# Kernel tuning notes

Measured on AMD Instinct MI355X. Metric: run time of the kernel, lower is better.

Reference implementation:

```python
import jax, jax.numpy as jnp
import numpy as np
import math

B, T, D_MODEL, H = 2, 2048, 768, 12
D = D_MODEL // H
EPS = 1e-8


def _l2norm(x, eps=EPS):
    # torch.nn.functional.normalize: x / max(||x||, eps)
    n = jnp.sqrt(jnp.sum(x * x, axis=-1, keepdims=True))
    return x / jnp.maximum(n, eps)


def setup_inputs() -> dict:
    key = jax.random.key(0)
    ks = jax.random.split(key, 7)
    sc = 1.0 / math.sqrt(D_MODEL)
    inp = {
        "query": jax.random.normal(ks[0], (B, T, D_MODEL), jnp.float32),
        "key": jax.random.normal(ks[1], (B, T, D_MODEL), jnp.float32),
        "value": jax.random.normal(ks[2], (B, T, D_MODEL), jnp.float32),
        "Wq": jax.random.normal(ks[3], (D_MODEL, D_MODEL), jnp.float32) * sc,
        "Wk": jax.random.normal(ks[4], (D_MODEL, D_MODEL), jnp.float32) * sc,
        "Wv": jax.random.normal(ks[5], (D_MODEL, D_MODEL), jnp.float32) * sc,
        "Wo": jax.random.normal(ks[6], (D_MODEL, D_MODEL), jnp.float32) * sc,
        "s_v": jnp.linspace(0.0, math.log(255.0), H).astype(jnp.float32),
        "s_r": jnp.zeros((H,), jnp.float32),
    }
    return inp


def reference(query, key, value, Wq, Wk, Wv, Wo, s_v, s_r):
    b, t, _ = query.shape

    def proj(x, W):  # Linear(bias=False) then split heads -> [B,H,T,D]
        return (x @ W.T).reshape(b, t, H, D).transpose(0, 2, 1, 3)

    q = _l2norm(proj(query, Wq))
    k = _l2norm(proj(key, Wk))
    v = _l2norm(proj(value, Wv))

    w = jnp.exp(s_v) + 1.0  # per-head decay exponent, in [2, 256]
    r = jnp.exp(s_r) + 1.0  # per-head scale

    # cosine-similarity scores in [-1, 1]
    s = jnp.einsum("bhqd,bhkd->bhqk", q, k)
    base = jnp.clip((s + 1.0) * 0.5, 0.0, 1.0)
    alpha = r[None, :, None, None] * jnp.power(base, w[None, :, None, None])

    # causal mask (no softmax normalization in screening attention)
    causal = jnp.tril(jnp.ones((t, t), dtype=bool))
    alpha = jnp.where(causal[None, None], alpha, 0.0)

    out = jnp.einsum("bhqk,bhkd->bhqd", alpha, v)  # [B,H,T,D]

    # TanhNorm: bound magnitude along head dim via tanh of the norm
    n = jnp.sqrt(jnp.sum(out * out, axis=-1, keepdims=True))
    out = jnp.tanh(n) * out / (n + EPS)

    out = out.transpose(0, 2, 1, 3).reshape(b, t, D_MODEL)
    return out @ Wo.T
```

## Files before the change

### kernel.cpp

```cpp
#include <hip/hip_runtime.h>
#include <hip/hip_bf16.h>
#include <math.h>


typedef __attribute__((ext_vector_type(8))) short short8;
typedef __attribute__((ext_vector_type(4))) float f32x4;
typedef __attribute__((ext_vector_type(4))) unsigned int uint4v;
typedef __attribute__((ext_vector_type(2))) unsigned int uint2v;
typedef __attribute__((ext_vector_type(4))) float float4v;

#define MFMA_BF16(a, b, c) __builtin_amdgcn_mfma_f32_16x16x32_bf16((a), (b), (c), 0, 0, 0)

static __device__ __forceinline__ unsigned short f2bf(float f) {
  union { float f; unsigned u; } v; v.f = f;
  unsigned r = v.u + 0x7FFFu + ((v.u >> 16) & 1u);
  return (unsigned short)(r >> 16);
}
static __device__ __forceinline__ unsigned pack2(float a, float b) {
  return (unsigned)f2bf(a) | ((unsigned)f2bf(b) << 16);
}
static __device__ __forceinline__ void gload_lds16(const void* g, void* l) {
  __builtin_amdgcn_global_load_lds((const __attribute__((address_space(1))) unsigned int*)g,
                                   (__attribute__((address_space(3))) unsigned int*)l, 16, 0, 0);
}

__global__ __launch_bounds__(256) void k_cvt(
    const float* __restrict__ s0, const float* __restrict__ s1, const float* __restrict__ s2,
    const float* __restrict__ s3, const float* __restrict__ s4, const float* __restrict__ s5,
    const float* __restrict__ s6, unsigned short* __restrict__ dst) {
  const size_t e = ((size_t)blockIdx.x * 256 + threadIdx.x) * 8;
  const float* src;
  size_t off;
  if (e < 9437184) {
    const int i = (int)(e / 3145728);
    src = (i == 0) ? s0 : (i == 1) ? s1 : s2;
    off = e - (size_t)i * 3145728;
  } else {
    const size_t ew = e - 9437184;
    const int i = (int)(ew / 589824);
    src = (i == 0) ? s3 : (i == 1) ? s4 : (i == 2) ? s5 : s6;
    off = ew - (size_t)i * 589824;
  }
  const float4v f0 = *(const float4v*)(src + off);
  const float4v f1 = *(const float4v*)(src + off + 4);
  uint4v u = {pack2(f0.x, f0.y), pack2(f0.z, f0.w), pack2(f1.x, f1.y), pack2(f1.z, f1.w)};
  *(uint4v*)(dst + e) = u;
}

__global__ __launch_bounds__(256) void k_proj(
    const unsigned short* __restrict__ Xb, const unsigned short* __restrict__ Wb,
    unsigned short* __restrict__ qb, unsigned short* __restrict__ kb,
    unsigned short* __restrict__ vtb) {
  __shared__ alignas(16) unsigned char smem[49152];
  float* o_s = (float*)smem;
  unsigned short* vt_s = (unsigned short*)smem;

  const int which = blockIdx.z;
  const int h = blockIdx.y;
  const unsigned short* X = Xb + (size_t)which * 3145728;
  const unsigned short* W = Wb + (size_t)which * 589824 + (size_t)h * 64 * 768;

  const int mbase = blockIdx.x * 128;
  const int tid = threadIdx.x;
  const int lane = tid & 63;
  const int wv = tid >> 6;
  const int wm = wv >> 1, wn = wv & 1;
  const int l15 = lane & 15, l4 = lane >> 4;
  const int srow8 = lane >> 3;
  const int schunk = (lane & 7) ^ srow8;

  f32x4 acc[4][2];
#pragma unroll
  for (int m = 0; m < 4; ++m)
#pragma unroll
    for (int n = 0; n < 2; ++n) acc[m][n] = (f32x4){0.f, 0.f, 0.f, 0.f};

#pragma unroll
  for (int i = 0; i < 4; ++i) {
    const int j = wv * 4 + i;
    gload_lds16(X + (size_t)(mbase + j * 8 + srow8) * 768 + schunk * 8, smem + j * 1024);
  }
#pragma unroll
  for (int i = 0; i < 2; ++i) {
    const int j = wv * 2 + i;
    gload_lds16(W + (size_t)(j * 8 + srow8) * 768 + schunk * 8, smem + 16384 + j * 1024);
  }

  for (int ks = 0; ks < 12; ++ks) {
    const int cur = (ks & 1) * 24576;
    asm volatile("s_waitcnt vmcnt(0)" ::: "memory");
    __builtin_amdgcn_sched_barrier(0);
    __builtin_amdgcn_s_barrier();
    __builtin_amdgcn_sched_barrier(0);
    if (ks < 11) {
      const int nxt = ((ks + 1) & 1) * 24576;
      const int k0n = (ks + 1) * 64;
#pragma unroll
      for (int i = 0; i < 4; ++i) {
        const int j = wv * 4 + i;
        gload_lds16(X + (size_t)(mbase + j * 8 + srow8) * 768 + k0n + schunk * 8,
                    smem + nxt + j * 1024);
      }
#pragma unroll
      for (int i = 0; i < 2; ++i) {
        const int j = wv * 2 + i;
        gload_lds16(W + (size_t)(j * 8 + srow8) * 768 + k0n + schunk * 8,
                    smem + nxt + 16384 + j * 1024);
      }
      __builtin_amdgcn_sched_barrier(0);
    }
    __builtin_amdgcn_s_setprio(1);
#pragma unroll
    for (int kc = 0; kc < 2; ++kc) {
      const int cx = (kc << 2) | l4;
      short8 ar[4], br[2];
#pragma unroll
      for (int m = 0; m < 4; ++m) {
        const int r = wm * 64 + m * 16 + l15;
        ar[m] = *(const short8*)(smem + cur + r * 128 + ((cx ^ (r & 7)) << 4));
      }
#pragma unroll
      for (int n = 0; n < 2; ++n) {
        const int r = wn * 32 + n * 16 + l15;
        br[n] = *(const short8*)(smem + cur + 16384 + r * 128 + ((cx ^ (r & 7)) << 4));
      }
#pragma unroll
      for (int m = 0; m < 4; ++m)
#pragma unroll
        for (int n = 0; n < 2; ++n) acc[m][n] = MFMA_BF16(ar[m], br[n], acc[m][n]);
    }
    __builtin_amdgcn_s_setprio(0);
  }

  const int b = mbase >> 11;
  const int tbase = mbase & 2047;
  const int bh = b * 12 + h;
  __syncthreads();
#pragma unroll
  for (int m = 0; m < 4; ++m)
#pragma unroll
    for (int n = 0; n < 2; ++n)
#pragma unroll
      for (int j = 0; j < 4; ++j)
        o_s[(wm * 64 + m * 16 + l4 * 4 + j) * 68 + wn * 32 + n * 16 + l15] = acc[m][n][j];
  __syncthreads();
  const int row2 = tid >> 1, half = tid & 1;
  float v[32];
  float ss = 0.f;
#pragma unroll
  for (int c = 0; c < 8; ++c) {
    float4v f = *(const float4v*)(o_s + row2 * 68 + half * 32 + c * 4);
    v[c * 4 + 0] = f.x; v[c * 4 + 1] = f.y; v[c * 4 + 2] = f.z; v[c * 4 + 3] = f.w;
    ss += f.x * f.x + f.y * f.y + f.z * f.z + f.w * f.w;
  }
  ss += __shfl_xor(ss, 1);
  const float inv = 1.f / fmaxf(sqrtf(ss), 1e-8f);
  if (which < 2) {
    unsigned short* outp =
        ((which == 0) ? qb : kb) + ((size_t)bh * 2048 + tbase + row2) * 64 + half * 32;
#pragma unroll
    for (int c = 0; c < 4; ++c) {
      uint4v o = {pack2(v[c * 8 + 0] * inv, v[c * 8 + 1] * inv),
                  pack2(v[c * 8 + 2] * inv, v[c * 8 + 3] * inv),
                  pack2(v[c * 8 + 4] * inv, v[c * 8 + 5] * inv),
                  pack2(v[c * 8 + 6] * inv, v[c * 8 + 7] * inv)};
      *(uint4v*)(outp + c * 8) = o;
    }
  } else {
    __syncthreads();
#pragma unroll
    for (int c = 0; c < 32; ++c)
      vt_s[(half * 32 + c) * 136 + row2] = f2bf(v[c] * inv);
    __syncthreads();
    const int d = tid >> 2, tc = (tid & 3) * 32;
    unsigned short* dst = vtb + ((size_t)bh * 64 + d) * 2048 + tbase + tc;
#pragma unroll
    for (int c = 0; c < 4; ++c)
      *(uint4v*)(dst + c * 8) = *(const uint4v*)(vt_s + d * 136 + tc + c * 8);
  }
}

__global__ __launch_bounds__(256) void k_attn(
    const unsigned short* __restrict__ qb, const unsigned short* __restrict__ kb,
    const unsigned short* __restrict__ vtb, const float* __restrict__ s_v,
    const float* __restrict__ s_r, unsigned short* __restrict__ attn) {
  __shared__ alignas(16) unsigned char smem[41984];
  unsigned short* p_s = (unsigned short*)(smem + 32768);
  float* o_s = (float*)smem;

  const int bid = blockIdx.x;
  const int ii = bid & 255, jj = bid >> 8;
  const int rank = (jj == 0) ? ii : (jj == 1) ? (511 - ii) : (512 + ii);
  const int qt = 31 - (rank / 24);
  const int bh = rank % 24;
  const int b = bh / 12, h = bh % 12;
  const int qbase = qt * 64;
  const unsigned short* Qp = qb + (size_t)bh * 2048 * 64;
  const unsigned short* Kp = kb + (size_t)bh * 2048 * 64;
  const unsigned short* VTp = vtb + (size_t)bh * 64 * 2048;

  const int tid = threadIdx.x;
  const int lane = tid & 63;
  const int wv = tid >> 6;
  const int wm = wv >> 1, wn = wv & 1;
  const int l15 = lane & 15, l4 = lane >> 4;
  const int srow8 = lane >> 3;
  const int schunk = (lane & 7) ^ srow8;

  const float w_h = expf(s_v[h]) + 1.0f;
  const float lr_h = log2f(expf(s_r[h]) + 1.0f);

#pragma unroll
  for (int i = 0; i < 2; ++i) {
    const int j = wv * 2 + i;
    gload_lds16(Kp + (size_t)(j * 8 + srow8) * 64 + schunk * 8, smem + j * 1024);
    gload_lds16(VTp + (size_t)(j * 8 + srow8) * 2048 + schunk * 8, smem + 16384 + j * 1024);
  }

  short8 qf[2][2];
#pragma unroll
  for (int n = 0; n < 2; ++n)
#pragma unroll
    for (int kc = 0; kc < 2; ++kc)
      qf[n][kc] = *(const short8*)(Qp + (size_t)(qbase + wn * 32 + n * 16 + l15) * 64 + kc * 32 +
                                   l4 * 8);

  f32x4 acc_o[2][2];
#pragma unroll
  for (int m = 0; m < 2; ++m)
#pragma unroll
    for (int n = 0; n < 2; ++n) acc_o[m][n] = (f32x4){0.f, 0.f, 0.f, 0.f};

  for (int kt = 0; kt <= qt; ++kt) {
    const int cur = (kt & 1) * 8192;
    asm volatile("s_waitcnt vmcnt(0)" ::: "memory");
    __builtin_amdgcn_sched_barrier(0);
    __builtin_amdgcn_s_barrier();
    __builtin_amdgcn_sched_barrier(0);
    if (kt < qt) {
      const int nxt = ((kt + 1) & 1) * 8192;
      const int kb2 = (kt + 1) * 64;
#pragma unroll
      for (int i = 0; i < 2; ++i) {
        const int j = wv * 2 + i;
        gload_lds16(Kp + (size_t)(kb2 + j * 8 + srow8) * 64 + schunk * 8, smem + nxt + j * 1024);
        gload_lds16(VTp + (size_t)(j * 8 + srow8) * 2048 + kb2 + schunk * 8,
                    smem + 16384 + nxt + j * 1024);
      }
      __builtin_amdgcn_sched_barrier(0);
    }
    f32x4 s_acc[2][2];
#pragma unroll
    for (int m = 0; m < 2; ++m)
#pragma unroll
      for (int n = 0; n < 2; ++n) s_acc[m][n] = (f32x4){0.f, 0.f, 0.f, 0.f};
    __builtin_amdgcn_s_setprio(1);
#pragma unroll
    for (int kc = 0; kc < 2; ++kc) {
      const int cx = (kc << 2) | l4;
      const int r0 = wm * 32 + l15, r1 = wm * 32 + 16 + l15;
      short8 a0 = *(const short8*)(smem + cur + r0 * 128 + ((cx ^ (r0 & 7)) << 4));
      short8 a1 = *(const short8*)(smem + cur + r1 * 128 + ((cx ^ (r1 & 7)) << 4));
      s_acc[0][0] = MFMA_BF16(a0, qf[0][kc], s_acc[0][0]);
      s_acc[0][1] = MFMA_BF16(a0, qf[1][kc], s_acc[0][1]);
      s_acc[1][0] = MFMA_BF16(a1, qf[0][kc], s_acc[1][0]);
      s_acc[1][1] = MFMA_BF16(a1, qf[1][kc], s_acc[1][1]);
    }
    __builtin_amdgcn_s_setprio(0);
    const bool diag = (kt == qt);
#pragma unroll
    for (int m = 0; m < 2; ++m)
#pragma unroll
      for (int n = 0; n < 2; ++n) {
        const int lkb = wm * 32 + m * 16 + l4 * 4;
        const int lq = wn * 32 + n * 16 + l15;
        float av[4];
#pragma unroll
        for (int t = 0; t < 4; ++t) {
          const float base = __builtin_amdgcn_fmed3f(fmaf(s_acc[m][n][t], 0.5f, 0.5f), 0.f, 1.f);
          float a = __builtin_amdgcn_exp2f(fmaf(w_h, __builtin_amdgcn_logf(base), lr_h));
          if (diag && (lkb + t) > lq) a = 0.f;
          av[t] = a;
        }
        uint2v u = {pack2(av[0], av[1]), pack2(av[2], av[3])};
        *(uint2v*)(p_s + lq * 72 + lkb) = u;
      }
    asm volatile("s_waitcnt lgkmcnt(0)" ::: "memory");
    __builtin_amdgcn_sched_barrier(0);
    __builtin_amdgcn_s_barrier();
    __builtin_amdgcn_sched_barrier(0);
    __builtin_amdgcn_s_setprio(1);
#pragma unroll
    for (int kc = 0; kc < 2; ++kc) {
      const int cx = (kc << 2) | l4;
      const int r0 = wm * 32 + l15, r1 = wm * 32 + 16 + l15;
      short8 pa0 = *(const short8*)(p_s + (wn * 32 + l15) * 72 + kc * 32 + l4 * 8);
      short8 pa1 = *(const short8*)(p_s + (wn * 32 + 16 + l15) * 72 + kc * 32 + l4 * 8);
      short8 vb0 = *(const short8*)(smem + 16384 + cur + r0 * 128 + ((cx ^ (r0 & 7)) << 4));
      short8 vb1 = *(const short8*)(smem + 16384 + cur + r1 * 128 + ((cx ^ (r1 & 7)) << 4));
      acc_o[0][0] = MFMA_BF16(pa0, vb0, acc_o[0][0]);
      acc_o[0][1] = MFMA_BF16(pa0, vb1, acc_o[0][1]);
      acc_o[1][0] = MFMA_BF16(pa1, vb0, acc_o[1][0]);
      acc_o[1][1] = MFMA_BF16(pa1, vb1, acc_o[1][1]);
    }
    __builtin_amdgcn_s_setprio(0);
  }
  __syncthreads();
#pragma unroll
  for (int qi = 0; qi < 2; ++qi)
#pragma unroll
    for (int di = 0; di < 2; ++di)
#pragma unroll
      for (int j = 0; j < 4; ++j)
        o_s[(wn * 32 + qi * 16 + l4 * 4 + j) * 68 + wm * 32 + di * 16 + l15] = acc_o[qi][di][j];
  __syncthreads();
  {
    const int row = tid >> 2, q4 = tid & 3;
    float vals[16];
    float ss = 0.f;
#pragma unroll
    for (int j = 0; j < 16; ++j) {
      vals[j] = o_s[row * 68 + q4 * 16 + j];
      ss += vals[j] * vals[j];
    }
    ss += __shfl_xor(ss, 1);
    ss += __shfl_xor(ss, 2);
    const float nrm = sqrtf(ss);
    const float sc = tanhf(nrm) / (nrm + 1e-8f);
    unsigned short* dst = attn + (size_t)(b * 2048 + qbase + row) * 768 + h * 64 + q4 * 16;
    uint4v o0 = {pack2(vals[0] * sc, vals[1] * sc), pack2(vals[2] * sc, vals[3] * sc),
                 pack2(vals[4] * sc, vals[5] * sc), pack2(vals[6] * sc, vals[7] * sc)};
    uint4v o1 = {pack2(vals[8] * sc, vals[9] * sc), pack2(vals[10] * sc, vals[11] * sc),
                 pack2(vals[12] * sc, vals[13] * sc), pack2(vals[14] * sc, vals[15] * sc)};
    *(uint4v*)(dst) = o0;
    *(uint4v*)(dst + 8) = o1;
  }
}

__global__ __launch_bounds__(256) void k_outproj(const unsigned short* __restrict__ attn,
                                                 const unsigned short* __restrict__ Wob,
                                                 float* __restrict__ out) {
  __shared__ alignas(16) unsigned char smem[49152];
  const int mbase = blockIdx.x * 128;
  const int nbase = blockIdx.y * 64;
  const int tid = threadIdx.x;
  const int lane = tid & 63;
  const int wv = tid >> 6;
  const int wm = wv >> 1, wn = wv & 1;
  const int l15 = lane & 15, l4 = lane >> 4;
  const int srow8 = lane >> 3;
  const int schunk = (lane & 7) ^ srow8;

  f32x4 acc[4][2];
#pragma unroll
  for (int m = 0; m < 4; ++m)
#pragma unroll
    for (int n = 0; n < 2; ++n) acc[m][n] = (f32x4){0.f, 0.f, 0.f, 0.f};

#pragma unroll
  for (int i = 0; i < 4; ++i) {
    const int j = wv * 4 + i;
    gload_lds16(attn + (size_t)(mbase + j * 8 + srow8) * 768 + schunk * 8, smem + j * 1024);
  }
#pragma unroll
  for (int i = 0; i < 2; ++i) {
    const int j = wv * 2 + i;
    gload_lds16(Wob + (size_t)(nbase + j * 8 + srow8) * 768 + schunk * 8,
                smem + 16384 + j * 1024);
  }

  for (int ks = 0; ks < 12; ++ks) {
    const int cur = (ks & 1) * 24576;
    asm volatile("s_waitcnt vmcnt(0)" ::: "memory");
    __builtin_amdgcn_sched_barrier(0);
    __builtin_amdgcn_s_barrier();
    __builtin_amdgcn_sched_barrier(0);
    if (ks < 11) {
      const int nxt = ((ks + 1) & 1) * 24576;
      const int k0n = (ks + 1) * 64;
#pragma unroll
      for (int i = 0; i < 4; ++i) {
        const int j = wv * 4 + i;
        gload_lds16(attn + (size_t)(mbase + j * 8 + srow8) * 768 + k0n + schunk * 8,
                    smem + nxt + j * 1024);
      }
#pragma unroll
      for (int i = 0; i < 2; ++i) {
        const int j = wv * 2 + i;
        gload_lds16(Wob + (size_t)(nbase + j * 8 + srow8) * 768 + k0n + schunk * 8,
                    smem + nxt + 16384 + j * 1024);
      }
      __builtin_amdgcn_sched_barrier(0);
    }
    __builtin_amdgcn_s_setprio(1);
#pragma unroll
    for (int kc = 0; kc < 2; ++kc) {
      const int cx = (kc << 2) | l4;
      short8 ar[4], br[2];
#pragma unroll
      for (int m = 0; m < 4; ++m) {
        const int r = wm * 64 + m * 16 + l15;
        ar[m] = *(const short8*)(smem + cur + r * 128 + ((cx ^ (r & 7)) << 4));
      }
#pragma unroll
      for (int n = 0; n < 2; ++n) {
        const int r = wn * 32 + n * 16 + l15;
        br[n] = *(const short8*)(smem + cur + 16384 + r * 128 + ((cx ^ (r & 7)) << 4));
      }
#pragma unroll
      for (int m = 0; m < 4; ++m)
#pragma unroll
        for (int n = 0; n < 2; ++n) acc[m][n] = MFMA_BF16(ar[m], br[n], acc[m][n]);
    }
    __builtin_amdgcn_s_setprio(0);
  }
#pragma unroll
  for (int m = 0; m < 4; ++m)
#pragma unroll
    for (int n = 0; n < 2; ++n)
#pragma unroll
      for (int j = 0; j < 4; ++j)
        out[(size_t)(mbase + wm * 64 + m * 16 + l4 * 4 + j) * 768 + nbase + wn * 32 + n * 16 +
            l15] = acc[m][n][j];
}

extern "C" void kernel_launch(void* const* d_in, const int* in_sizes, int n_in, void* d_out,
                              int out_size, void* d_ws, size_t ws_size, hipStream_t stream) {
  (void)in_sizes;
  (void)n_in;
  (void)out_size;
  (void)ws_size;
  const float* query = (const float*)d_in[0];
  const float* key = (const float*)d_in[1];
  const float* value = (const float*)d_in[2];
  const float* Wq = (const float*)d_in[3];
  const float* Wk = (const float*)d_in[4];
  const float* Wv = (const float*)d_in[5];
  const float* Wo = (const float*)d_in[6];
  const float* s_v = (const float*)d_in[7];
  const float* s_r = (const float*)d_in[8];
  float* out = (float*)d_out;

  unsigned short* cvt = (unsigned short*)d_ws;
  unsigned short* Xb = cvt;
  unsigned short* Wb = cvt + 9437184;
  unsigned short* qb = cvt + 11796480;
  unsigned short* kb = qb + 3145728;
  unsigned short* vtb = kb + 3145728;
  unsigned short* attn = cvt;

  k_cvt<<<5760, 256, 0, stream>>>(query, key, value, Wq, Wk, Wv, Wo, cvt);
  k_proj<<<dim3(32, 12, 3), 256, 0, stream>>>(Xb, Wb, qb, kb, vtb);
  k_attn<<<dim3(768), 256, 0, stream>>>(qb, kb, vtb, s_v, s_r, attn);
  k_outproj<<<dim3(32, 12), 256, 0, stream>>>(attn, Wb + 3 * 589824, out);
}
```

Baseline: 82.63 us.

## Split attention tile across eight waves instead of four

Raises the attention kernel block from 256 to 512 threads and gives each wave a 32x16 sub-tile instead of 32x32, so every wave issues half as many MFMAs and exp/log evaluations per key tile. The goal is more waves per CU, to hide LDS and exp latency and shorten the serial per-block chain on the causal workload. The cost is more barrier participants, lower per-wave reuse of K/V fragments loaded from LDS, and a different epilogue split (eight threads per row with an extra shuffle).

```diff
diff --git a/kernel.cpp b/kernel.cpp
--- a/kernel.cpp
+++ b/kernel.cpp
@@ -180,7 +180,7 @@
   }
 }
 
-__global__ __launch_bounds__(256) void k_attn(
+__global__ __launch_bounds__(512) void k_attn(
     const unsigned short* __restrict__ qb, const unsigned short* __restrict__ kb,
     const unsigned short* __restrict__ vtb, const float* __restrict__ s_v,
     const float* __restrict__ s_r, unsigned short* __restrict__ attn) {
@@ -202,7 +202,7 @@
   const int tid = threadIdx.x;
   const int lane = tid & 63;
   const int wv = tid >> 6;
-  const int wm = wv >> 1, wn = wv & 1;
+  const int wm = wv >> 2, wn = wv & 3;
   const int l15 = lane & 15, l4 = lane >> 4;
   const int srow8 = lane >> 3;
   const int schunk = (lane & 7) ^ srow8;
@@ -210,26 +210,17 @@
   const float w_h = expf(s_v[h]) + 1.0f;
   const float lr_h = log2f(expf(s_r[h]) + 1.0f);
 
-#pragma unroll
-  for (int i = 0; i < 2; ++i) {
-    const int j = wv * 2 + i;
-    gload_lds16(Kp + (size_t)(j * 8 + srow8) * 64 + schunk * 8, smem + j * 1024);
-    gload_lds16(VTp + (size_t)(j * 8 + srow8) * 2048 + schunk * 8, smem + 16384 + j * 1024);
-  }
-
-  short8 qf[2][2];
-#pragma unroll
-  for (int n = 0; n < 2; ++n)
-#pragma unroll
-    for (int kc = 0; kc < 2; ++kc)
-      qf[n][kc] = *(const short8*)(Qp + (size_t)(qbase + wn * 32 + n * 16 + l15) * 64 + kc * 32 +
-                                   l4 * 8);
-
-  f32x4 acc_o[2][2];
-#pragma unroll
-  for (int m = 0; m < 2; ++m)
-#pragma unroll
-    for (int n = 0; n < 2; ++n) acc_o[m][n] = (f32x4){0.f, 0.f, 0.f, 0.f};
+  gload_lds16(Kp + (size_t)(wv * 8 + srow8) * 64 + schunk * 8, smem + wv * 1024);
+  gload_lds16(VTp + (size_t)(wv * 8 + srow8) * 2048 + schunk * 8, smem + 16384 + wv * 1024);
+
+  short8 qf[2];
+#pragma unroll
+  for (int kc = 0; kc < 2; ++kc)
+    qf[kc] = *(const short8*)(Qp + (size_t)(qbase + wn * 16 + l15) * 64 + kc * 32 + l4 * 8);
+
+  f32x4 acc_o[2];
+#pragma unroll
+  for (int m = 0; m < 2; ++m) acc_o[m] = (f32x4){0.f, 0.f, 0.f, 0.f};
 
   for (int kt = 0; kt <= qt; ++kt) {
     const int cur = (kt & 1) * 8192;
@@ -240,20 +231,14 @@
     if (kt < qt) {
       const int nxt = ((kt + 1) & 1) * 8192;
       const int kb2 = (kt + 1) * 64;
-#pragma unroll
-      for (int i = 0; i < 2; ++i) {
-        const int j = wv * 2 + i;
-        gload_lds16(Kp + (size_t)(kb2 + j * 8 + srow8) * 64 + schunk * 8, smem + nxt + j * 1024);
-        gload_lds16(VTp + (size_t)(j * 8 + srow8) * 2048 + kb2 + schunk * 8,
-                    smem + 16384 + nxt + j * 1024);
-      }
+      gload_lds16(Kp + (size_t)(kb2 + wv * 8 + srow8) * 64 + schunk * 8, smem + nxt + wv * 1024);
+      gload_lds16(VTp + (size_t)(wv * 8 + srow8) * 2048 + kb2 + schunk * 8,
+                  smem + 16384 + nxt + wv * 1024);
       __builtin_amdgcn_sched_barrier(0);
     }
-    f32x4 s_acc[2][2];
-#pragma unroll
-    for (int m = 0; m < 2; ++m)
-#pragma unroll
-      for (int n = 0; n < 2; ++n) s_acc[m][n] = (f32x4){0.f, 0.f, 0.f, 0.f};
+    f32x4 s_acc[2];
+#pragma unroll
+    for (int m = 0; m < 2; ++m) s_acc[m] = (f32x4){0.f, 0.f, 0.f, 0.f};
     __builtin_amdgcn_s_setprio(1);
 #pragma unroll
     for (int kc = 0; kc < 2; ++kc) {
@@ -261,30 +246,26 @@
       const int r0 = wm * 32 + l15, r1 = wm * 32 + 16 + l15;
       short8 a0 = *(const short8*)(smem + cur + r0 * 128 + ((cx ^ (r0 & 7)) << 4));
       short8 a1 = *(const short8*)(smem + cur + r1 * 128 + ((cx ^ (r1 & 7)) << 4));
-      s_acc[0][0] = MFMA_BF16(a0, qf[0][kc], s_acc[0][0]);
-      s_acc[0][1] = MFMA_BF16(a0, qf[1][kc], s_acc[0][1]);
-      s_acc[1][0] = MFMA_BF16(a1, qf[0][kc], s_acc[1][0]);
-      s_acc[1][1] = MFMA_BF16(a1, qf[1][kc], s_acc[1][1]);
+      s_acc[0] = MFMA_BF16(a0, qf[kc], s_acc[0]);
+      s_acc[1] = MFMA_BF16(a1, qf[kc], s_acc[1]);
     }
     __builtin_amdgcn_s_setprio(0);
     const bool diag = (kt == qt);
 #pragma unroll
-    for (int m = 0; m < 2; ++m)
-#pragma unroll
-      for (int n = 0; n < 2; ++n) {
-        const int lkb = wm * 32 + m * 16 + l4 * 4;
-        const int lq = wn * 32 + n * 16 + l15;
-        float av[4];
-#pragma unroll
-        for (int t = 0; t < 4; ++t) {
-          const float base = __builtin_amdgcn_fmed3f(fmaf(s_acc[m][n][t], 0.5f, 0.5f), 0.f, 1.f);
-          float a = __builtin_amdgcn_exp2f(fmaf(w_h, __builtin_amdgcn_logf(base), lr_h));
-          if (diag && (lkb + t) > lq) a = 0.f;
-          av[t] = a;
-        }
-        uint2v u = {pack2(av[0], av[1]), pack2(av[2], av[3])};
-        *(uint2v*)(p_s + lq * 72 + lkb) = u;
-      }
+    for (int m = 0; m < 2; ++m) {
+      const int lkb = wm * 32 + m * 16 + l4 * 4;
+      const int lq = wn * 16 + l15;
+      float av[4];
+#pragma unroll
+      for (int t = 0; t < 4; ++t) {
+        const float base = __builtin_amdgcn_fmed3f(fmaf(s_acc[m][t], 0.5f, 0.5f), 0.f, 1.f);
+        float a = __builtin_amdgcn_exp2f(fmaf(w_h, __builtin_amdgcn_logf(base), lr_h));
+        if (diag && (lkb + t) > lq) a = 0.f;
+        av[t] = a;
+      }
+      uint2v u = {pack2(av[0], av[1]), pack2(av[2], av[3])};
+      *(uint2v*)(p_s + lq * 72 + lkb) = u;
+    }
     asm volatile("s_waitcnt lgkmcnt(0)" ::: "memory");
     __builtin_amdgcn_sched_barrier(0);
     __builtin_amdgcn_s_barrier();
@@ -294,46 +275,40 @@
     for (int kc = 0; kc < 2; ++kc) {
       const int cx = (kc << 2) | l4;
       const int r0 = wm * 32 + l15, r1 = wm * 32 + 16 + l15;
-      short8 pa0 = *(const short8*)(p_s + (wn * 32 + l15) * 72 + kc * 32 + l4 * 8);
-      short8 pa1 = *(const short8*)(p_s + (wn * 32 + 16 + l15) * 72 + kc * 32 + l4 * 8);
+      short8 pa = *(const short8*)(p_s + (wn * 16 + l15) * 72 + kc * 32 + l4 * 8);
       short8 vb0 = *(const short8*)(smem + 16384 + cur + r0 * 128 + ((cx ^ (r0 & 7)) << 4));
       short8 vb1 = *(const short8*)(smem + 16384 + cur + r1 * 128 + ((cx ^ (r1 & 7)) << 4));
-      acc_o[0][0] = MFMA_BF16(pa0, vb0, acc_o[0][0]);
-      acc_o[0][1] = MFMA_BF16(pa0, vb1, acc_o[0][1]);
-      acc_o[1][0] = MFMA_BF16(pa1, vb0, acc_o[1][0]);
-      acc_o[1][1] = MFMA_BF16(pa1, vb1, acc_o[1][1]);
+      acc_o[0] = MFMA_BF16(pa, vb0, acc_o[0]);
+      acc_o[1] = MFMA_BF16(pa, vb1, acc_o[1]);
     }
     __builtin_amdgcn_s_setprio(0);
   }
   __syncthreads();
 #pragma unroll
-  for (int qi = 0; qi < 2; ++qi)
-#pragma unroll
-    for (int di = 0; di < 2; ++di)
-#pragma unroll
-      for (int j = 0; j < 4; ++j)
-        o_s[(wn * 32 + qi * 16 + l4 * 4 + j) * 68 + wm * 32 + di * 16 + l15] = acc_o[qi][di][j];
+  for (int m = 0; m < 2; ++m)
+#pragma unroll
+    for (int j = 0; j < 4; ++j)
+      o_s[(wn * 16 + l4 * 4 + j) * 68 + wm * 32 + m * 16 + l15] = acc_o[m][j];
   __syncthreads();
   {
-    const int row = tid >> 2, q4 = tid & 3;
-    float vals[16];
+    const int row = tid >> 3, d8 = (tid & 7) * 8;
+    float vals[8];
     float ss = 0.f;
 #pragma unroll
-    for (int j = 0; j < 16; ++j) {
-      vals[j] = o_s[row * 68 + q4 * 16 + j];
-      ss += vals[j] * vals[j];
+    for (int c = 0; c < 2; ++c) {
+      float4v f = *(const float4v*)(o_s + row * 68 + d8 + c * 4);
+      vals[c * 4 + 0] = f.x; vals[c * 4 + 1] = f.y; vals[c * 4 + 2] = f.z; vals[c * 4 + 3] = f.w;
+      ss += f.x * f.x + f.y * f.y + f.z * f.z + f.w * f.w;
     }
     ss += __shfl_xor(ss, 1);
     ss += __shfl_xor(ss, 2);
+    ss += __shfl_xor(ss, 4);
     const float nrm = sqrtf(ss);
     const float sc = tanhf(nrm) / (nrm + 1e-8f);
-    unsigned short* dst = attn + (size_t)(b * 2048 + qbase + row) * 768 + h * 64 + q4 * 16;
-    uint4v o0 = {pack2(vals[0] * sc, vals[1] * sc), pack2(vals[2] * sc, vals[3] * sc),
-                 pack2(vals[4] * sc, vals[5] * sc), pack2(vals[6] * sc, vals[7] * sc)};
-    uint4v o1 = {pack2(vals[8] * sc, vals[9] * sc), pack2(vals[10] * sc, vals[11] * sc),
-                 pack2(vals[12] * sc, vals[13] * sc), pack2(vals[14] * sc, vals[15] * sc)};
-    *(uint4v*)(dst) = o0;
-    *(uint4v*)(dst + 8) = o1;
+    unsigned short* dst = attn + (size_t)(b * 2048 + qbase + row) * 768 + h * 64 + d8;
+    uint4v o = {pack2(vals[0] * sc, vals[1] * sc), pack2(vals[2] * sc, vals[3] * sc),
+                pack2(vals[4] * sc, vals[5] * sc), pack2(vals[6] * sc, vals[7] * sc)};
+    *(uint4v*)(dst) = o;
   }
 }
 
@@ -451,6 +426,6 @@
 
   k_cvt<<<5760, 256, 0, stream>>>(query, key, value, Wq, Wk, Wv, Wo, cvt);
   k_proj<<<dim3(32, 12, 3), 256, 0, stream>>>(Xb, Wb, qb, kb, vtb);
-  k_attn<<<dim3(768), 256, 0, stream>>>(qb, kb, vtb, s_v, s_r, attn);
+  k_attn<<<dim3(768), 512, 0, stream>>>(qb, kb, vtb, s_v, s_r, attn);
   k_outproj<<<dim3(32, 12), 256, 0, stream>>>(attn, Wb + 3 * 589824, out);
 }
```

New measurement: 80.54 us. -2.5%, faster.
